# Optimization experiments

Hardware: AMD Instinct MI355X
Metric: run time of the kernel (lower is better)

## Reference

```python
import jax, jax.numpy as jnp
import numpy as np

HEADS = 8
DIM_HEAD = 32
GROUPS = 8
EPS = 1e-5


def setup_inputs() -> dict:
    key = jax.random.key(0)
    k0, k1, k2 = jax.random.split(key, 3)
    dim = 256
    inner = HEADS * DIM_HEAD  # 256
    x = jax.random.normal(k0, (1, dim, 16, 16, 16), dtype=jnp.float32)
    gn_weight = jnp.ones((dim,), dtype=jnp.float32)
    gn_bias = jnp.zeros((dim,), dtype=jnp.float32)
    w_qkv = jax.random.normal(k1, (3 * inner, dim), dtype=jnp.float32) * 0.02
    w_out = jax.random.normal(k2, (dim, inner), dtype=jnp.float32) * 0.02
    b_out = jnp.zeros((dim,), dtype=jnp.float32)
    return {"x": x, "gn_weight": gn_weight, "gn_bias": gn_bias,
            "w_qkv": w_qkv, "w_out": w_out, "b_out": b_out}


def reference(x, gn_weight, gn_bias, w_qkv, w_out, b_out):
    b, c, d, h, w = x.shape
    n = d * h * w  # tokens

    # --- GroupNorm(8, c) with affine ---
    xg = x.reshape(b, GROUPS, c // GROUPS, n)
    mean = xg.mean(axis=(2, 3), keepdims=True)
    var = xg.var(axis=(2, 3), keepdims=True)
    xn = ((xg - mean) * jax.lax.rsqrt(var + EPS)).reshape(b, c, n)
    xn = xn * gn_weight[:, None] + gn_bias[:, None]

    # --- 1x1 Conv3d QKV projection (no bias) ---
    qkv = jnp.einsum('bcn,oc->bon', xn, w_qkv)              # (b, 3*H*dh, n)
    qkv = qkv.reshape(b, 3, HEADS, DIM_HEAD, n)
    q, k, v = qkv[:, 0], qkv[:, 1], qkv[:, 2]               # each (b, H, dh, n)

    # --- naive softmax attention over n = d*h*w tokens ---
    scale = DIM_HEAD ** (-0.5)
    sim = jnp.einsum('bhdi,bhdj->bhij', q, k) * scale       # (b, H, n, n)
    attn = jax.nn.softmax(sim, axis=-1)
    out = jnp.einsum('bhij,bhdj->bhdi', attn, v)            # (b, H, dh, n)
    out = out.reshape(b, HEADS * DIM_HEAD, n)

    # --- 1x1 Conv3d output projection (with bias) ---
    y = jnp.einsum('bcn,oc->bon', out, w_out) + b_out[:, None]
    return y.reshape(b, c, d, h, w)
```

## Files before the change

kernel.cpp:

```cpp
#include <hip/hip_runtime.h>
#include <hip/hip_bf16.h>
#include <math.h>


typedef __attribute__((ext_vector_type(8))) short bf16x8;
typedef __attribute__((ext_vector_type(4))) short bf16x4;
typedef __attribute__((ext_vector_type(4))) float f32x4;
typedef __attribute__((ext_vector_type(4))) unsigned short u16x4;

__device__ inline unsigned short f2bf(float f) {
  __hip_bfloat16 h = __float2bfloat16(f);
  return *reinterpret_cast<unsigned short*>(&h);
}

__global__ __launch_bounds__(256) void xt_gn_kernel(const float* __restrict__ x,
                                                    unsigned short* __restrict__ xTb,
                                                    float2* __restrict__ psum2) {
  __shared__ float tile[64][65];
  __shared__ float red[4][4];
  int nb = blockIdx.x * 64, cb = blockIdx.y * 64;
  int tn = threadIdx.x & 63, t4 = threadIdx.x >> 6;
  float slo = 0.f, qlo = 0.f, shi = 0.f, qhi = 0.f;
#pragma unroll
  for (int i = 0; i < 16; ++i) {
    int cc = t4 + i * 4;
    float v = x[(size_t)(cb + cc) * 4096 + nb + tn];
    tile[cc][tn] = v;
    if (i < 8) { slo += v; qlo += v * v; } else { shi += v; qhi += v * v; }
  }
#pragma unroll
  for (int off = 32; off > 0; off >>= 1) {
    slo += __shfl_down(slo, off); qlo += __shfl_down(qlo, off);
    shi += __shfl_down(shi, off); qhi += __shfl_down(qhi, off);
  }
  if ((threadIdx.x & 63) == 0) {
    red[t4][0] = slo; red[t4][1] = qlo; red[t4][2] = shi; red[t4][3] = qhi;
  }
  __syncthreads();
  if (threadIdx.x == 0) {
    float a = (red[0][0] + red[1][0]) + (red[2][0] + red[3][0]);
    float b = (red[0][1] + red[1][1]) + (red[2][1] + red[3][1]);
    psum2[(blockIdx.y * 2) * 64 + blockIdx.x] = make_float2(a, b);
  } else if (threadIdx.x == 64) {
    float a = (red[0][2] + red[1][2]) + (red[2][2] + red[3][2]);
    float b = (red[0][3] + red[1][3]) + (red[2][3] + red[3][3]);
    psum2[(blockIdx.y * 2 + 1) * 64 + blockIdx.x] = make_float2(a, b);
  }
#pragma unroll
  for (int i = 0; i < 16; ++i) {
    int nn = t4 + i * 4;
    xTb[(size_t)(nb + nn) * 256 + cb + tn] = f2bf(tile[tn][nn]);
  }
}

__global__ __launch_bounds__(256) void fold_all_kernel(const float* __restrict__ w_qkv,
                                                       const float* __restrict__ gnw,
                                                       const float* __restrict__ gnb,
                                                       const float2* __restrict__ psum2,
                                                       const float* __restrict__ w_out,
                                                       unsigned short* __restrict__ w2b,
                                                       float* __restrict__ bias0,
                                                       unsigned short* __restrict__ w_outb) {
  int bid = blockIdx.x;
  int t = threadIdx.x;
  if (bid >= 192) {
    int i = ((bid - 192) * 256 + t) * 4;
    float4 v = *(const float4*)(w_out + i);
    u16x4 o;
    o[0] = f2bf(v.x); o[1] = f2bf(v.y); o[2] = f2bf(v.z); o[3] = f2bf(v.w);
    *(u16x4*)(w_outb + i) = o;
    return;
  }
  __shared__ float sm[8], sr[8];
  __shared__ float s_al[256], s_be[256];
  {
    int g = t >> 5, ii = t & 31;
    float2 p0 = psum2[g * 64 + ii];
    float2 p1 = psum2[g * 64 + 32 + ii];
    float s = p0.x + p1.x, q = p0.y + p1.y;
#pragma unroll
    for (int off = 16; off > 0; off >>= 1) {
      s += __shfl_xor(s, off);
      q += __shfl_xor(q, off);
    }
    if (ii == 0) {
      float mean = s * (1.f / 131072.f);
      float var = q * (1.f / 131072.f) - mean * mean;
      sm[g] = mean;
      sr[g] = rsqrtf(var + 1e-5f);
    }
  }
  __syncthreads();
  {
    int c = t, gg = c >> 5;
    float mean = sm[gg], rstd = sr[gg];
    float al = rstd * gnw[c];
    s_al[c] = al;
    s_be[c] = gnb[c] - mean * al;
  }
  __syncthreads();
  int w = t >> 6, lane = t & 63;
  int row = bid * 4 + w;
  float4 v = *(const float4*)(w_qkv + row * 256 + lane * 4);
  int c0 = lane * 4;
  float part = (v.x * s_be[c0] + v.y * s_be[c0 + 1]) +
               (v.z * s_be[c0 + 2] + v.w * s_be[c0 + 3]);
  u16x4 o;
  o[0] = f2bf(v.x * s_al[c0]);
  o[1] = f2bf(v.y * s_al[c0 + 1]);
  o[2] = f2bf(v.z * s_al[c0 + 2]);
  o[3] = f2bf(v.w * s_al[c0 + 3]);
  *(u16x4*)(w2b + row * 256 + c0) = o;
#pragma unroll
  for (int off = 32; off > 0; off >>= 1) part += __shfl_down(part, off);
  if (lane == 0) bias0[row] = part;
}

__global__ __launch_bounds__(256) void gemm_qkv_mfma(const unsigned short* __restrict__ w2b,
                                                     const unsigned short* __restrict__ xTb,
                                                     const float* __restrict__ bias0,
                                                     unsigned short* __restrict__ qt,
                                                     unsigned short* __restrict__ ktb,
                                                     unsigned short* __restrict__ v16) {
  const int nb = blockIdx.x, mb = blockIdx.y;
  const int t = threadIdx.x;
  const int w = t >> 6, lane = t & 63;
  const int c = lane & 15, g = lane >> 4;
  const int m0 = mb * 64 + w * 16;
  const int n0 = nb * 64;
  const f32x4 zero4 = {0.f, 0.f, 0.f, 0.f};

  const unsigned short* ap = w2b + (size_t)(m0 + c) * 256 + g * 8;
  bf16x8 af[8];
#pragma unroll
  for (int ks = 0; ks < 8; ++ks) af[ks] = *(const bf16x8*)(ap + ks * 32);

  f32x4 acc[4] = {zero4, zero4, zero4, zero4};
  const unsigned short* bp = xTb + (size_t)(n0 + c) * 256 + g * 8;
#pragma unroll
  for (int half = 0; half < 2; ++half) {
    bf16x8 bf[4][4];
#pragma unroll
    for (int nt = 0; nt < 4; ++nt)
#pragma unroll
      for (int k2 = 0; k2 < 4; ++k2)
        bf[nt][k2] = *(const bf16x8*)(bp + (size_t)nt * 4096 + half * 128 + k2 * 32);
#pragma unroll
    for (int k2 = 0; k2 < 4; ++k2)
#pragma unroll
      for (int nt = 0; nt < 4; ++nt)
        acc[nt] = __builtin_amdgcn_mfma_f32_16x16x32_bf16(af[half * 4 + k2], bf[nt][k2],
                                                          acc[nt], 0, 0, 0);
  }

  const int o0 = m0 + g * 4;
  const int t3 = o0 >> 8;
  const int h = (o0 >> 5) & 7;
  const int d0 = o0 & 31;
  float b4[4];
#pragma unroll
  for (int r = 0; r < 4; ++r) b4[r] = bias0[o0 + r];
  const float qs = 0.17677669529663687f * 1.4426950408889634f;
#pragma unroll
  for (int nt = 0; nt < 4; ++nt) {
    int n = n0 + nt * 16 + c;
    if (t3 == 0) {
      u16x4 v;
#pragma unroll
      for (int r = 0; r < 4; ++r) v[r] = f2bf((acc[nt][r] + b4[r]) * qs);
      *(u16x4*)(qt + (size_t)(h * 4096 + n) * 32 + d0) = v;
    } else if (t3 == 1) {
      u16x4 v;
#pragma unroll
      for (int r = 0; r < 4; ++r) v[r] = f2bf(acc[nt][r] + b4[r]);
      *(u16x4*)(ktb + (size_t)(h * 4096 + n) * 32 + d0) = v;
    } else {
#pragma unroll
      for (int r = 0; r < 4; ++r)
        v16[(size_t)((h * 256 + (n >> 4)) * 32 + d0 + r) * 16 + (n & 15)] =
            f2bf(acc[nt][r] + b4[r]);
    }
  }
}

__device__ __forceinline__ void attn_step(const bf16x8* kf, const bf16x4 vf[2][4],
                                          const bf16x8* qf, f32x4 (*oacc)[2],
                                          f32x4* lones) {
  const f32x4 zero4 = {0.f, 0.f, 0.f, 0.f};
  const short one_bf = (short)0x3F80;
  const bf16x4 onesv = {one_bf, one_bf, one_bf, one_bf};
#pragma unroll
  for (int it = 0; it < 4; ++it) {
    f32x4 st[4];
    __builtin_amdgcn_s_setprio(1);
#pragma unroll
    for (int js = 0; js < 4; ++js)
      st[js] = __builtin_amdgcn_mfma_f32_16x16x32_bf16(kf[js], qf[it], zero4, 0, 0, 0);
    __builtin_amdgcn_s_setprio(0);
    bf16x4 pb[4];
#pragma unroll
    for (int js = 0; js < 4; ++js) {
      unsigned u0 = __float_as_uint(__builtin_amdgcn_exp2f(st[js][0]));
      unsigned u1 = __float_as_uint(__builtin_amdgcn_exp2f(st[js][1]));
      unsigned u2 = __float_as_uint(__builtin_amdgcn_exp2f(st[js][2]));
      unsigned u3 = __float_as_uint(__builtin_amdgcn_exp2f(st[js][3]));
      union { unsigned u[2]; bf16x4 v; } pu;
      pu.u[0] = (u0 >> 16) | (u1 & 0xFFFF0000u);
      pu.u[1] = (u2 >> 16) | (u3 & 0xFFFF0000u);
      pb[js] = pu.v;
    }
    __builtin_amdgcn_s_setprio(1);
#pragma unroll
    for (int js = 0; js < 4; ++js) {
      oacc[it][0] = __builtin_amdgcn_mfma_f32_16x16x16bf16_1k(vf[0][js], pb[js], oacc[it][0], 0, 0, 0);
      oacc[it][1] = __builtin_amdgcn_mfma_f32_16x16x16bf16_1k(vf[1][js], pb[js], oacc[it][1], 0, 0, 0);
      lones[it] = __builtin_amdgcn_mfma_f32_16x16x16bf16_1k(onesv, pb[js], lones[it], 0, 0, 0);
    }
    __builtin_amdgcn_s_setprio(0);
  }
}

__global__ __launch_bounds__(512, 1) void attn_mfma_kernel(const unsigned short* __restrict__ qt,
                                                           const unsigned short* __restrict__ ktb,
                                                           const unsigned short* __restrict__ v16,
                                                           unsigned short* __restrict__ outTb) {
  const int b = blockIdx.x;
  const int h = b >> 6;
  const int i0 = (b & 63) * 64;
  const int t = threadIdx.x;
  const int w = t >> 6;
  const int lane = t & 63;
  const int c = lane & 15;
  const int g = lane >> 4;
  const f32x4 zero4 = {0.f, 0.f, 0.f, 0.f};

  const unsigned short* qb = qt + (size_t)h * 131072 + (size_t)(i0 + c) * 32 + g * 8;
  bf16x8 qf[4];
#pragma unroll
  for (int it = 0; it < 4; ++it) qf[it] = *(const bf16x8*)(qb + it * 512);

  const unsigned short* kp = ktb + (size_t)h * 131072 + (size_t)(w * 512 + c) * 32 + g * 8;
  const unsigned short* vp = v16 + (size_t)((h * 256 + w * 32) * 32 + c) * 16 + g * 4;

  f32x4 lones[4] = {zero4, zero4, zero4, zero4};
  f32x4 oacc[4][2];
#pragma unroll
  for (int it = 0; it < 4; ++it) {
    oacc[it][0] = zero4;
    oacc[it][1] = zero4;
  }

#define KLOAD(dst, tt)                                         \
  _Pragma("unroll") for (int js = 0; js < 4; ++js)             \
      dst[js] = *(const bf16x8*)(kp + (tt) * 2048 + js * 512);
#define VLOAD(dst, tt)                                                        \
  _Pragma("unroll") for (int dh = 0; dh < 2; ++dh)                            \
      _Pragma("unroll") for (int js = 0; js < 4; ++js)                        \
          dst[dh][js] = *(const bf16x4*)(vp + ((tt) * 4 + js) * 512 + dh * 256);

  bf16x8 kfA[4], kfB[4];
  bf16x4 vfA[2][4], vfB[2][4];
  KLOAD(kfA, 0);
  VLOAD(vfA, 0);

#pragma unroll 1
  for (int jt2 = 0; jt2 < 4; ++jt2) {
    const int base = jt2 * 2;
    KLOAD(kfB, base + 1);
    VLOAD(vfB, base + 1);
    attn_step(kfA, vfA, qf, oacc, lones);
    if (jt2 < 3) {
      KLOAD(kfA, base + 2);
      VLOAD(vfA, base + 2);
    }
    attn_step(kfB, vfB, qf, oacc, lones);
  }
#undef KLOAD
#undef VLOAD

  __shared__ float lds_o[8][2][4][4][17];
  __shared__ float lds_l[8][4][16];
#pragma unroll
  for (int it = 0; it < 4; ++it) {
    if (g == 0) lds_l[w][it][c] = lones[it][0];
  }
#pragma unroll 1
  for (int itc = 0; itc < 4; ++itc) {
#pragma unroll
    for (int dh = 0; dh < 2; ++dh)
#pragma unroll
      for (int r = 0; r < 4; ++r)
        lds_o[w][dh][g][r][c] = oacc[itc][dh][r];
    __syncthreads();
    if (w < 2) {
      const int dh = w;
      float L = ((lds_l[0][itc][c] + lds_l[1][itc][c]) + (lds_l[2][itc][c] + lds_l[3][itc][c])) +
                ((lds_l[4][itc][c] + lds_l[5][itc][c]) + (lds_l[6][itc][c] + lds_l[7][itc][c]));
      float inv = 1.f / L;
      u16x4 o;
#pragma unroll
      for (int r = 0; r < 4; ++r) {
        float v = ((lds_o[0][dh][g][r][c] + lds_o[1][dh][g][r][c]) +
                   (lds_o[2][dh][g][r][c] + lds_o[3][dh][g][r][c])) +
                  ((lds_o[4][dh][g][r][c] + lds_o[5][dh][g][r][c]) +
                   (lds_o[6][dh][g][r][c] + lds_o[7][dh][g][r][c]));
        o[r] = f2bf(v * inv);
      }
      *(u16x4*)(outTb + (size_t)(i0 + itc * 16 + c) * 256 + h * 32 + dh * 16 + g * 4) = o;
    }
    __syncthreads();
  }
}

__global__ __launch_bounds__(256) void gemm_out_mfma(const unsigned short* __restrict__ w_outb,
                                                     const unsigned short* __restrict__ outTb,
                                                     const float* __restrict__ bias,
                                                     float* __restrict__ y) {
  const int nb = blockIdx.x, mb = blockIdx.y;
  const int t = threadIdx.x;
  const int w = t >> 6, lane = t & 63;
  const int c = lane & 15, g = lane >> 4;
  const int m0 = mb * 64 + w * 16;
  const int n0 = nb * 64;
  const f32x4 zero4 = {0.f, 0.f, 0.f, 0.f};

  const unsigned short* ap = w_outb + (size_t)(m0 + c) * 256 + g * 8;
  bf16x8 af[8];
#pragma unroll
  for (int ks = 0; ks < 8; ++ks) af[ks] = *(const bf16x8*)(ap + ks * 32);

  f32x4 acc[4] = {zero4, zero4, zero4, zero4};
  const unsigned short* bp = outTb + (size_t)(n0 + c) * 256 + g * 8;
#pragma unroll
  for (int half = 0; half < 2; ++half) {
    bf16x8 bf[4][4];
#pragma unroll
    for (int nt = 0; nt < 4; ++nt)
#pragma unroll
      for (int k2 = 0; k2 < 4; ++k2)
        bf[nt][k2] = *(const bf16x8*)(bp + (size_t)nt * 4096 + half * 128 + k2 * 32);
#pragma unroll
    for (int k2 = 0; k2 < 4; ++k2)
#pragma unroll
      for (int nt = 0; nt < 4; ++nt)
        acc[nt] = __builtin_amdgcn_mfma_f32_16x16x32_bf16(af[half * 4 + k2], bf[nt][k2],
                                                          acc[nt], 0, 0, 0);
  }

  const int o0 = m0 + g * 4;
  float b4[4];
#pragma unroll
  for (int r = 0; r < 4; ++r) b4[r] = bias[o0 + r];
#pragma unroll
  for (int nt = 0; nt < 4; ++nt) {
    int n = n0 + nt * 16 + c;
#pragma unroll
    for (int r = 0; r < 4; ++r)
      y[(size_t)(o0 + r) * 4096 + n] = acc[nt][r] + b4[r];
  }
}

extern "C" void kernel_launch(void* const* d_in, const int* in_sizes, int n_in,
                              void* d_out, int out_size, void* d_ws, size_t ws_size,
                              hipStream_t stream) {
  const float* x = (const float*)d_in[0];
  const float* gnw = (const float*)d_in[1];
  const float* gnb = (const float*)d_in[2];
  const float* w_qkv = (const float*)d_in[3];
  const float* w_out = (const float*)d_in[4];
  const float* b_out = (const float*)d_in[5];
  float* ws = (float*)d_ws;

  float2* psum2 = (float2*)ws;
  float* bias0 = ws + 1088;
  unsigned short* w2b = (unsigned short*)(ws + 2048);
  unsigned short* w_outb = w2b + 196608;
  unsigned short* xTb = w_outb + 65536;
  unsigned short* qt = xTb + 1048576;
  unsigned short* ktb = qt + 1048576;
  unsigned short* v16 = ktb + 1048576;
  unsigned short* outTb = v16 + 1048576;
  float* y = (float*)d_out;

  hipLaunchKernelGGL(xt_gn_kernel, dim3(64, 4), dim3(256), 0, stream, x, xTb, psum2);
  hipLaunchKernelGGL(fold_all_kernel, dim3(256), dim3(256), 0, stream, w_qkv, gnw, gnb,
                     psum2, w_out, w2b, bias0, w_outb);
  hipLaunchKernelGGL(gemm_qkv_mfma, dim3(64, 12), dim3(256), 0, stream, w2b, xTb, bias0, qt, ktb, v16);
  hipLaunchKernelGGL(attn_mfma_kernel, dim3(512), dim3(512), 0, stream, qt, ktb, v16, outTb);
  hipLaunchKernelGGL(gemm_out_mfma, dim3(64, 4), dim3(256), 0, stream, w_outb, outTb, b_out, y);
}
```

Baseline: 69.79 us.

## Fold GroupNorm weight prep into QKV GEMM and pair attention score tiles

Removes the separate fold kernel. The QKV GEMM now computes GroupNorm statistics, scales w_qkv by the affine factors, converts it to bf16 and computes the folded bias per block. The output GEMM converts w_out to bf16 inline. This saves one launch and a global round trip, but every QKV block redoes the stats and a serial 256-length bias dot product. Separately, the attention step now issues the score MFMAs for two query tiles before doing the exp, giving more independent work to interleave at the cost of higher register pressure.

```diff
diff --git a/kernel.cpp b/kernel.cpp
--- a/kernel.cpp
+++ b/kernel.cpp
@@ -53,72 +53,11 @@
   }
 }
 
-__global__ __launch_bounds__(256) void fold_all_kernel(const float* __restrict__ w_qkv,
-                                                       const float* __restrict__ gnw,
-                                                       const float* __restrict__ gnb,
-                                                       const float2* __restrict__ psum2,
-                                                       const float* __restrict__ w_out,
-                                                       unsigned short* __restrict__ w2b,
-                                                       float* __restrict__ bias0,
-                                                       unsigned short* __restrict__ w_outb) {
-  int bid = blockIdx.x;
-  int t = threadIdx.x;
-  if (bid >= 192) {
-    int i = ((bid - 192) * 256 + t) * 4;
-    float4 v = *(const float4*)(w_out + i);
-    u16x4 o;
-    o[0] = f2bf(v.x); o[1] = f2bf(v.y); o[2] = f2bf(v.z); o[3] = f2bf(v.w);
-    *(u16x4*)(w_outb + i) = o;
-    return;
-  }
-  __shared__ float sm[8], sr[8];
-  __shared__ float s_al[256], s_be[256];
-  {
-    int g = t >> 5, ii = t & 31;
-    float2 p0 = psum2[g * 64 + ii];
-    float2 p1 = psum2[g * 64 + 32 + ii];
-    float s = p0.x + p1.x, q = p0.y + p1.y;
-#pragma unroll
-    for (int off = 16; off > 0; off >>= 1) {
-      s += __shfl_xor(s, off);
-      q += __shfl_xor(q, off);
-    }
-    if (ii == 0) {
-      float mean = s * (1.f / 131072.f);
-      float var = q * (1.f / 131072.f) - mean * mean;
-      sm[g] = mean;
-      sr[g] = rsqrtf(var + 1e-5f);
-    }
-  }
-  __syncthreads();
-  {
-    int c = t, gg = c >> 5;
-    float mean = sm[gg], rstd = sr[gg];
-    float al = rstd * gnw[c];
-    s_al[c] = al;
-    s_be[c] = gnb[c] - mean * al;
-  }
-  __syncthreads();
-  int w = t >> 6, lane = t & 63;
-  int row = bid * 4 + w;
-  float4 v = *(const float4*)(w_qkv + row * 256 + lane * 4);
-  int c0 = lane * 4;
-  float part = (v.x * s_be[c0] + v.y * s_be[c0 + 1]) +
-               (v.z * s_be[c0 + 2] + v.w * s_be[c0 + 3]);
-  u16x4 o;
-  o[0] = f2bf(v.x * s_al[c0]);
-  o[1] = f2bf(v.y * s_al[c0 + 1]);
-  o[2] = f2bf(v.z * s_al[c0 + 2]);
-  o[3] = f2bf(v.w * s_al[c0 + 3]);
-  *(u16x4*)(w2b + row * 256 + c0) = o;
-#pragma unroll
-  for (int off = 32; off > 0; off >>= 1) part += __shfl_down(part, off);
-  if (lane == 0) bias0[row] = part;
-}
-
-__global__ __launch_bounds__(256) void gemm_qkv_mfma(const unsigned short* __restrict__ w2b,
+__global__ __launch_bounds__(256) void gemm_qkv_mfma(const float* __restrict__ w_qkv,
                                                      const unsigned short* __restrict__ xTb,
-                                                     const float* __restrict__ bias0,
+                                                     const float* __restrict__ gnw,
+                                                     const float* __restrict__ gnb,
+                                                     const float2* __restrict__ psum2,
                                                      unsigned short* __restrict__ qt,
                                                      unsigned short* __restrict__ ktb,
                                                      unsigned short* __restrict__ v16) {
@@ -130,10 +69,65 @@
   const int n0 = nb * 64;
   const f32x4 zero4 = {0.f, 0.f, 0.f, 0.f};
 
-  const unsigned short* ap = w2b + (size_t)(m0 + c) * 256 + g * 8;
+  __shared__ float sm[8], sr[8];
+  __shared__ float s_al[256], s_be[256];
+  __shared__ float bias_s[64];
+  {
+    int gg = t >> 5, ii = t & 31;
+    float2 p0 = psum2[gg * 64 + ii];
+    float2 p1 = psum2[gg * 64 + 32 + ii];
+    float s = p0.x + p1.x, q = p0.y + p1.y;
+#pragma unroll
+    for (int off = 16; off > 0; off >>= 1) {
+      s += __shfl_xor(s, off);
+      q += __shfl_xor(q, off);
+    }
+    if (ii == 0) {
+      float mean = s * (1.f / 131072.f);
+      float var = q * (1.f / 131072.f) - mean * mean;
+      sm[gg] = mean;
+      sr[gg] = rsqrtf(var + 1e-5f);
+    }
+  }
+  __syncthreads();
+  {
+    int cc = t, gg = cc >> 5;
+    float mean = sm[gg], rstd = sr[gg];
+    float al = rstd * gnw[cc];
+    s_al[cc] = al;
+    s_be[cc] = gnb[cc] - mean * al;
+  }
+  __syncthreads();
+  if (t < 64) {
+    int row = mb * 64 + t;
+    const float* wr = w_qkv + (size_t)row * 256;
+    float sum = 0.f;
+#pragma unroll 8
+    for (int k = 0; k < 256; k += 4) {
+      float4 v = *(const float4*)(wr + k);
+      sum += (v.x * s_be[k] + v.y * s_be[k + 1]) + (v.z * s_be[k + 2] + v.w * s_be[k + 3]);
+    }
+    bias_s[t] = sum;
+  }
+  const float* ap = w_qkv + (size_t)(m0 + c) * 256 + g * 8;
   bf16x8 af[8];
 #pragma unroll
-  for (int ks = 0; ks < 8; ++ks) af[ks] = *(const bf16x8*)(ap + ks * 32);
+  for (int ks = 0; ks < 8; ++ks) {
+    float4 a0 = *(const float4*)(ap + ks * 32);
+    float4 a1 = *(const float4*)(ap + ks * 32 + 4);
+    int e0 = ks * 32 + g * 8;
+    bf16x8 v;
+    v[0] = (short)f2bf(a0.x * s_al[e0 + 0]);
+    v[1] = (short)f2bf(a0.y * s_al[e0 + 1]);
+    v[2] = (short)f2bf(a0.z * s_al[e0 + 2]);
+    v[3] = (short)f2bf(a0.w * s_al[e0 + 3]);
+    v[4] = (short)f2bf(a1.x * s_al[e0 + 4]);
+    v[5] = (short)f2bf(a1.y * s_al[e0 + 5]);
+    v[6] = (short)f2bf(a1.z * s_al[e0 + 6]);
+    v[7] = (short)f2bf(a1.w * s_al[e0 + 7]);
+    af[ks] = v;
+  }
+  __syncthreads();
 
   f32x4 acc[4] = {zero4, zero4, zero4, zero4};
   const unsigned short* bp = xTb + (size_t)(n0 + c) * 256 + g * 8;
@@ -159,7 +153,7 @@
   const int d0 = o0 & 31;
   float b4[4];
 #pragma unroll
-  for (int r = 0; r < 4; ++r) b4[r] = bias0[o0 + r];
+  for (int r = 0; r < 4; ++r) b4[r] = bias_s[w * 16 + g * 4 + r];
   const float qs = 0.17677669529663687f * 1.4426950408889634f;
 #pragma unroll
   for (int nt = 0; nt < 4; ++nt) {
@@ -190,31 +184,40 @@
   const short one_bf = (short)0x3F80;
   const bf16x4 onesv = {one_bf, one_bf, one_bf, one_bf};
 #pragma unroll
-  for (int it = 0; it < 4; ++it) {
-    f32x4 st[4];
+  for (int ip = 0; ip < 2; ++ip) {
+    f32x4 st[2][4];
     __builtin_amdgcn_s_setprio(1);
 #pragma unroll
-    for (int js = 0; js < 4; ++js)
-      st[js] = __builtin_amdgcn_mfma_f32_16x16x32_bf16(kf[js], qf[it], zero4, 0, 0, 0);
+    for (int i2 = 0; i2 < 2; ++i2)
+#pragma unroll
+      for (int js = 0; js < 4; ++js)
+        st[i2][js] = __builtin_amdgcn_mfma_f32_16x16x32_bf16(kf[js], qf[ip * 2 + i2],
+                                                             zero4, 0, 0, 0);
     __builtin_amdgcn_s_setprio(0);
-    bf16x4 pb[4];
-#pragma unroll
-    for (int js = 0; js < 4; ++js) {
-      unsigned u0 = __float_as_uint(__builtin_amdgcn_exp2f(st[js][0]));
-      unsigned u1 = __float_as_uint(__builtin_amdgcn_exp2f(st[js][1]));
-      unsigned u2 = __float_as_uint(__builtin_amdgcn_exp2f(st[js][2]));
-      unsigned u3 = __float_as_uint(__builtin_amdgcn_exp2f(st[js][3]));
-      union { unsigned u[2]; bf16x4 v; } pu;
-      pu.u[0] = (u0 >> 16) | (u1 & 0xFFFF0000u);
-      pu.u[1] = (u2 >> 16) | (u3 & 0xFFFF0000u);
-      pb[js] = pu.v;
-    }
+    bf16x4 pb[2][4];
+#pragma unroll
+    for (int i2 = 0; i2 < 2; ++i2)
+#pragma unroll
+      for (int js = 0; js < 4; ++js) {
+        unsigned u0 = __float_as_uint(__builtin_amdgcn_exp2f(st[i2][js][0]));
+        unsigned u1 = __float_as_uint(__builtin_amdgcn_exp2f(st[i2][js][1]));
+        unsigned u2 = __float_as_uint(__builtin_amdgcn_exp2f(st[i2][js][2]));
+        unsigned u3 = __float_as_uint(__builtin_amdgcn_exp2f(st[i2][js][3]));
+        union { unsigned u[2]; bf16x4 v; } pu;
+        pu.u[0] = (u0 >> 16) | (u1 & 0xFFFF0000u);
+        pu.u[1] = (u2 >> 16) | (u3 & 0xFFFF0000u);
+        pb[i2][js] = pu.v;
+      }
     __builtin_amdgcn_s_setprio(1);
 #pragma unroll
-    for (int js = 0; js < 4; ++js) {
-      oacc[it][0] = __builtin_amdgcn_mfma_f32_16x16x16bf16_1k(vf[0][js], pb[js], oacc[it][0], 0, 0, 0);
-      oacc[it][1] = __builtin_amdgcn_mfma_f32_16x16x16bf16_1k(vf[1][js], pb[js], oacc[it][1], 0, 0, 0);
-      lones[it] = __builtin_amdgcn_mfma_f32_16x16x16bf16_1k(onesv, pb[js], lones[it], 0, 0, 0);
+    for (int i2 = 0; i2 < 2; ++i2) {
+      const int it = ip * 2 + i2;
+#pragma unroll
+      for (int js = 0; js < 4; ++js) {
+        oacc[it][0] = __builtin_amdgcn_mfma_f32_16x16x16bf16_1k(vf[0][js], pb[i2][js], oacc[it][0], 0, 0, 0);
+        oacc[it][1] = __builtin_amdgcn_mfma_f32_16x16x16bf16_1k(vf[1][js], pb[i2][js], oacc[it][1], 0, 0, 0);
+        lones[it] = __builtin_amdgcn_mfma_f32_16x16x16bf16_1k(onesv, pb[i2][js], lones[it], 0, 0, 0);
+      }
     }
     __builtin_amdgcn_s_setprio(0);
   }
@@ -312,7 +315,7 @@
   }
 }
 
-__global__ __launch_bounds__(256) void gemm_out_mfma(const unsigned short* __restrict__ w_outb,
+__global__ __launch_bounds__(256) void gemm_out_mfma(const float* __restrict__ w_out,
                                                      const unsigned short* __restrict__ outTb,
                                                      const float* __restrict__ bias,
                                                      float* __restrict__ y) {
@@ -324,10 +327,19 @@
   const int n0 = nb * 64;
   const f32x4 zero4 = {0.f, 0.f, 0.f, 0.f};
 
-  const unsigned short* ap = w_outb + (size_t)(m0 + c) * 256 + g * 8;
+  const float* ap = w_out + (size_t)(m0 + c) * 256 + g * 8;
   bf16x8 af[8];
 #pragma unroll
-  for (int ks = 0; ks < 8; ++ks) af[ks] = *(const bf16x8*)(ap + ks * 32);
+  for (int ks = 0; ks < 8; ++ks) {
+    float4 a0 = *(const float4*)(ap + ks * 32);
+    float4 a1 = *(const float4*)(ap + ks * 32 + 4);
+    bf16x8 v;
+    v[0] = (short)f2bf(a0.x); v[1] = (short)f2bf(a0.y);
+    v[2] = (short)f2bf(a0.z); v[3] = (short)f2bf(a0.w);
+    v[4] = (short)f2bf(a1.x); v[5] = (short)f2bf(a1.y);
+    v[6] = (short)f2bf(a1.z); v[7] = (short)f2bf(a1.w);
+    af[ks] = v;
+  }
 
   f32x4 acc[4] = {zero4, zero4, zero4, zero4};
   const unsigned short* bp = outTb + (size_t)(n0 + c) * 256 + g * 8;
@@ -372,10 +384,7 @@
   float* ws = (float*)d_ws;
 
   float2* psum2 = (float2*)ws;
-  float* bias0 = ws + 1088;
-  unsigned short* w2b = (unsigned short*)(ws + 2048);
-  unsigned short* w_outb = w2b + 196608;
-  unsigned short* xTb = w_outb + 65536;
+  unsigned short* xTb = (unsigned short*)(ws + 2048);
   unsigned short* qt = xTb + 1048576;
   unsigned short* ktb = qt + 1048576;
   unsigned short* v16 = ktb + 1048576;
@@ -383,9 +392,8 @@
   float* y = (float*)d_out;
 
   hipLaunchKernelGGL(xt_gn_kernel, dim3(64, 4), dim3(256), 0, stream, x, xTb, psum2);
-  hipLaunchKernelGGL(fold_all_kernel, dim3(256), dim3(256), 0, stream, w_qkv, gnw, gnb,
-                     psum2, w_out, w2b, bias0, w_outb);
-  hipLaunchKernelGGL(gemm_qkv_mfma, dim3(64, 12), dim3(256), 0, stream, w2b, xTb, bias0, qt, ktb, v16);
+  hipLaunchKernelGGL(gemm_qkv_mfma, dim3(64, 12), dim3(256), 0, stream, w_qkv, xTb,
+                     gnw, gnb, psum2, qt, ktb, v16);
   hipLaunchKernelGGL(attn_mfma_kernel, dim3(512), dim3(512), 0, stream, qt, ktb, v16, outTb);
-  hipLaunchKernelGGL(gemm_out_mfma, dim3(64, 4), dim3(256), 0, stream, w_outb, outTb, b_out, y);
-}
+  hipLaunchKernelGGL(gemm_out_mfma, dim3(64, 4), dim3(256), 0, stream, w_out, outTb, b_out, y);
+}
```

Result: slower. 75.10 us (+7.6%).
